# Kernel tuning notes

Measured on AMD Instinct MI355X. Metric: run time of the kernel, lower is better.

## Reference

```python
import jax, jax.numpy as jnp
import numpy as np

EMB = 1024
HEADS = 16
HEAD_SIZE = EMB // HEADS
B, T = 2, 2048


def setup_inputs() -> dict:
    key = jax.random.key(0)
    k1, k2, k3 = jax.random.split(key, 3)
    scale = 0.02
    x = jax.random.normal(k1, (B, T, EMB), dtype=jnp.float32)
    w_qkv = jax.random.normal(k2, (3 * EMB, EMB), dtype=jnp.float32) * scale  # torch Linear weight [out,in]
    w_out = jax.random.normal(k3, (EMB, EMB), dtype=jnp.float32) * scale
    return {"x": x, "w_qkv": w_qkv, "w_out": w_out}


def reference(x, w_qkv, w_out):
    Bx, Tx, C = x.shape
    att_scale = 1.0 / np.sqrt(HEAD_SIZE).astype(np.float32)
    qkv = x @ w_qkv.T  # [B,T,3C]
    q, k, v = jnp.split(qkv, 3, axis=-1)
    # [B,T,H,Dh] -> [B,H,T,Dh]
    q = q.reshape(Bx, Tx, HEADS, HEAD_SIZE).transpose(0, 2, 1, 3)
    k = k.reshape(Bx, Tx, HEADS, HEAD_SIZE).transpose(0, 2, 1, 3)
    v = v.reshape(Bx, Tx, HEADS, HEAD_SIZE).transpose(0, 2, 1, 3)
    att = jnp.einsum('bhqd,bhkd->bhqk', q, k) * att_scale
    causal = jnp.tril(jnp.ones((Tx, Tx), dtype=bool))  # True = keep
    att = jnp.where(causal[None, None], att, jnp.finfo(att.dtype).min)
    att = jax.nn.softmax(att, axis=-1)
    y = jnp.einsum('bhqk,bhkd->bhqd', att, v)
    y = y.transpose(0, 2, 1, 3).reshape(Bx, Tx, C)
    return y @ w_out.T
```

## Files before the change

### kernel.cpp

```cpp
#include <hip/hip_runtime.h>
#include <hip/hip_bf16.h>
#include <cstdint>


typedef __bf16 bf16x8 __attribute__((ext_vector_type(8)));
typedef float  f32x4  __attribute__((ext_vector_type(4)));
typedef unsigned short u16x4 __attribute__((ext_vector_type(4)));

#define EMB   1024
#define HEADS 16
#define HD    64
#define TT    2048
#define NROWS 4096
#define QKVN  3072
#define SCL   0.18033688f
#define THR   11.0f

__global__ void cvt_all(const float* __restrict__ x, const float* __restrict__ wq,
                        const float* __restrict__ wo, __bf16* __restrict__ xb,
                        __bf16* __restrict__ wqb, __bf16* __restrict__ wob) {
  const int bid = blockIdx.x;
  const float* in; __bf16* out; int i;
  if (bid < 2048)      { in = x;  out = xb;  i = bid * 256 + threadIdx.x; }
  else if (bid < 3584) { in = wq; out = wqb; i = (bid - 2048) * 256 + threadIdx.x; }
  else                 { in = wo; out = wob; i = (bid - 3584) * 256 + threadIdx.x; }
  const float4* p = (const float4*)in + (size_t)i * 2;
  float4 a = p[0], b = p[1];
  bf16x8 o;
  o[0] = (__bf16)a.x; o[1] = (__bf16)a.y; o[2] = (__bf16)a.z; o[3] = (__bf16)a.w;
  o[4] = (__bf16)b.x; o[5] = (__bf16)b.y; o[6] = (__bf16)b.z; o[7] = (__bf16)b.w;
  *((bf16x8*)out + i) = o;
}

__device__ __forceinline__ void gload_lds16(const void* g, void* l) {
  __builtin_amdgcn_global_load_lds(
      (const __attribute__((address_space(1))) void*)(uintptr_t)g,
      (__attribute__((address_space(3))) void*)(uint32_t)(uintptr_t)l,
      16, 0, 0);
}

template <int MODE>
__global__ __launch_bounds__(256, 2)
void gemm_bt(const __bf16* __restrict__ A, const __bf16* __restrict__ Bm,
             void* __restrict__ Cout, __bf16* __restrict__ vt,
             int M, int N, int K) {
  __shared__ __align__(16) char As[128 * 128];
  __shared__ __align__(16) char Bs[128 * 128];
  const int tid  = threadIdx.x;
  const int lane = tid & 63;
  const int wid  = tid >> 6;
  const int wr = wid >> 1, wc = wid & 1;
  const int nwg = gridDim.x * gridDim.y;
  int flat = blockIdx.y * gridDim.x + blockIdx.x;
  flat = (flat & 7) * (nwg >> 3) + (flat >> 3);
  const int brow = (flat / gridDim.x) * 128;
  const int bcol = (flat % gridDim.x) * 128;
  const int fr = lane & 15, g = lane >> 4;

  f32x4 acc[4][4];
#pragma unroll
  for (int m = 0; m < 4; m++)
#pragma unroll
    for (int n = 0; n < 4; n++)
#pragma unroll
      for (int r = 0; r < 4; r++) acc[m][n][r] = 0.0f;

  for (int k0 = 0; k0 < K; k0 += 64) {
    __syncthreads();
#pragma unroll
    for (int i = 0; i < 4; i++) {
      const int c = tid + i * 256;
      const int row = c >> 3, pos = c & 7;
      const int sc = pos ^ (row & 7);
      gload_lds16(A  + (size_t)(brow + row) * K + k0 + sc * 8, As + c * 16);
      gload_lds16(Bm + (size_t)(bcol + row) * K + k0 + sc * 8, Bs + c * 16);
    }
    __syncthreads();

    bf16x8 af[4][2], bfr[4][2];
#pragma unroll
    for (int m = 0; m < 4; m++)
#pragma unroll
      for (int kc = 0; kc < 2; kc++) {
        const int row = wr * 64 + m * 16 + fr;
        af[m][kc] = *(const bf16x8*)(As + row * 128 + (((kc << 2) | g) ^ (fr & 7)) * 16);
      }
#pragma unroll
    for (int n = 0; n < 4; n++)
#pragma unroll
      for (int kc = 0; kc < 2; kc++) {
        const int row = wc * 64 + n * 16 + fr;
        bfr[n][kc] = *(const bf16x8*)(Bs + row * 128 + (((kc << 2) | g) ^ (fr & 7)) * 16);
      }
#pragma unroll
    for (int kc = 0; kc < 2; kc++)
#pragma unroll
      for (int m = 0; m < 4; m++)
#pragma unroll
        for (int n = 0; n < 4; n++)
          acc[m][n] = __builtin_amdgcn_mfma_f32_16x16x32_bf16(af[m][kc], bfr[n][kc], acc[m][n], 0, 0, 0);
  }

  const int rbase = brow + wr * 64 + g * 4;
  const int cbase = bcol + wc * 64 + fr;
  if (MODE == 0) {
#pragma unroll
    for (int m = 0; m < 4; m++)
#pragma unroll
      for (int n = 0; n < 4; n++) {
        const int col = cbase + n * 16;
#pragma unroll
        for (int r = 0; r < 4; r++)
          ((float*)Cout)[(size_t)(rbase + m * 16 + r) * N + col] = acc[m][n][r];
      }
  } else if (bcol < 2 * EMB) {
    const float qscale = (bcol < EMB) ? SCL : 1.0f;
#pragma unroll
    for (int m = 0; m < 4; m++)
#pragma unroll
      for (int n = 0; n < 4; n++) {
        const int col = cbase + n * 16;
#pragma unroll
        for (int r = 0; r < 4; r++)
          ((__bf16*)Cout)[(size_t)(rbase + m * 16 + r) * N + col] = (__bf16)(acc[m][n][r] * qscale);
      }
  } else {
#pragma unroll
    for (int m = 0; m < 4; m++) {
      const int row0 = rbase + m * 16;
      const int b = row0 >> 11, t0 = row0 & 2047;
#pragma unroll
      for (int n = 0; n < 4; n++) {
        const int vcol = cbase + n * 16 - 2 * EMB;
        const int bh = b * HEADS + (vcol >> 6);
        const int d  = vcol & 63;
        u16x4 pk;
#pragma unroll
        for (int r = 0; r < 4; r++) {
          const __bf16 h = (__bf16)acc[m][n][r];
          pk[r] = *(const unsigned short*)&h;
        }
        *(u16x4*)(vt + ((size_t)bh * HD + d) * TT + t0) = pk;
      }
    }
  }
}

__device__ __forceinline__ int psw(int row) {
  return (((row & 7) ^ ((row >> 3) & 7))) << 4;
}

__global__ __launch_bounds__(256, 2)
void attn_causal9(const __bf16* __restrict__ qkv, const __bf16* __restrict__ vt,
                  __bf16* __restrict__ yb) {
  __shared__ __align__(16) char Kbuf[4][8192];
  __shared__ __align__(16) char Vbuf[4][8192];
  __shared__ __align__(16) char Pbuf[4][2048];

  const int tid = threadIdx.x;
  const int lane = tid & 63, w = tid >> 6;
  const int L = blockIdx.x;
  const int bh = L & 31;
  const int chunk = 31 - (L >> 5);
  const int b = bh >> 4, h = bh & 15;
  const size_t rowbase = (size_t)b * TT;
  const int q0 = chunk * 64 + w * 16;
  const int fr = lane & 15, g = lane >> 4;
  const int ntiles = chunk + 1;

  bf16x8 qf[2];
#pragma unroll
  for (int kc = 0; kc < 2; kc++)
    qf[kc] = *(const bf16x8*)(qkv + (rowbase + q0 + fr) * QKVN + h * HD + kc * 32 + g * 8);

  bf16x8 ones;
#pragma unroll
  for (int j = 0; j < 8; j++) ones[j] = (__bf16)1.0f;

  f32x4 o[4];
  f32x4 lacc;
  float m[4];
#pragma unroll
  for (int n = 0; n < 4; n++)
#pragma unroll
    for (int r = 0; r < 4; r++) o[n][r] = 0.0f;
#pragma unroll
  for (int r = 0; r < 4; r++) { lacc[r] = 0.0f; m[r] = -1e30f; }

  auto stageKV = [&](int kt, int buf) {
#pragma unroll
    for (int i = 0; i < 2; i++) {
      const int c = tid + i * 256;
      const int row = c >> 3;
      const int c16 = (c & 7) ^ (row & 7);
      gload_lds16(qkv + (rowbase + kt * 64 + row) * QKVN + EMB + h * HD + c16 * 8,
                  Kbuf[buf] + c * 16);
    }
#pragma unroll
    for (int i = 0; i < 2; i++) {
      const int c = tid + i * 256;
      const int row = c >> 3;
      const int c16 = (c & 7) ^ (row & 7);
      gload_lds16(vt + ((size_t)bh * HD + row) * TT + kt * 64 + c16 * 8,
                  Vbuf[buf] + c * 16);
    }
  };

  auto doQK = [&](int kt, f32x4 (&s)[4]) {
    const char* Kc = Kbuf[kt & 3];
    bf16x8 kf[4][2];
#pragma unroll
    for (int n = 0; n < 4; n++)
#pragma unroll
      for (int kc = 0; kc < 2; kc++) {
        const int row = n * 16 + fr;
        kf[n][kc] = *(const bf16x8*)(Kc + row * 128 + (((kc << 2) | g) ^ (row & 7)) * 16);
      }
#pragma unroll
    for (int n = 0; n < 4; n++) {
#pragma unroll
      for (int r = 0; r < 4; r++) s[n][r] = 0.0f;
#pragma unroll
      for (int kc = 0; kc < 2; kc++)
        s[n] = __builtin_amdgcn_mfma_f32_16x16x32_bf16(qf[kc], kf[n][kc], s[n], 0, 0, 0);
    }
  };

  auto doSoftmax = [&](int kt, f32x4 (&s)[4]) {
    const int kv0 = kt * 64;
    if (kt == chunk) {
#pragma unroll
      for (int n = 0; n < 4; n++)
#pragma unroll
        for (int r = 0; r < 4; r++) {
          const int qg = q0 + g * 4 + r;
          const int kg = kv0 + n * 16 + fr;
          if (kg > qg) s[n][r] = -1e30f;
        }
    }
    float pm[4];
#pragma unroll
    for (int r = 0; r < 4; r++)
      pm[r] = fmaxf(fmaxf(s[0][r], s[1][r]), fmaxf(s[2][r], s[3][r]));
    const bool ok = (pm[0] <= m[0] + THR) && (pm[1] <= m[1] + THR) &&
                    (pm[2] <= m[2] + THR) && (pm[3] <= m[3] + THR);
    if (!__all(ok)) {
#pragma unroll
      for (int r = 0; r < 4; r++) {
        float rm = pm[r];
#pragma unroll
        for (int d = 1; d < 16; d <<= 1) rm = fmaxf(rm, __shfl_xor(rm, d, 16));
        const float nm = fmaxf(m[r], rm);
        const float f = __builtin_amdgcn_exp2f(m[r] - nm);
        m[r] = nm;
        lacc[r] *= f;
#pragma unroll
        for (int n = 0; n < 4; n++) o[n][r] *= f;
      }
    }
#pragma unroll
    for (int n = 0; n < 4; n++)
#pragma unroll
      for (int r = 0; r < 4; r++) {
        const float e = __builtin_amdgcn_exp2f(s[n][r] - m[r]);
        const int row = g * 4 + r;
        *(__bf16*)(Pbuf[w] + row * 128 + (((n * 16 + fr) * 2) ^ psw(row))) = (__bf16)e;
      }
  };

  auto doPV = [&](int kt) {
    const char* Vc = Vbuf[kt & 3];
    bf16x8 pa[2];
#pragma unroll
    for (int kc = 0; kc < 2; kc++)
      pa[kc] = *(const bf16x8*)(Pbuf[w] + fr * 128 + ((kc * 64 + g * 16) ^ psw(fr)));
    bf16x8 vb[4][2];
#pragma unroll
    for (int n = 0; n < 4; n++)
#pragma unroll
      for (int kc = 0; kc < 2; kc++) {
        const int row = n * 16 + fr;
        vb[n][kc] = *(const bf16x8*)(Vc + row * 128 + (((kc << 2) | g) ^ (row & 7)) * 16);
      }
#pragma unroll
    for (int kc = 0; kc < 2; kc++) {
      lacc = __builtin_amdgcn_mfma_f32_16x16x32_bf16(pa[kc], ones, lacc, 0, 0, 0);
#pragma unroll
      for (int n = 0; n < 4; n++)
        o[n] = __builtin_amdgcn_mfma_f32_16x16x32_bf16(pa[kc], vb[n][kc], o[n], 0, 0, 0);
    }
  };

  stageKV(0, 0);
  if (ntiles > 1) stageKV(1, 1);
  if (ntiles > 2) stageKV(2, 2);
  if (ntiles > 2) asm volatile("s_waitcnt vmcnt(4)" ::: "memory");
  else            asm volatile("s_waitcnt vmcnt(0)" ::: "memory");
  __builtin_amdgcn_s_barrier();

  {
    f32x4 s0[4];
    doQK(0, s0);
    doSoftmax(0, s0);
  }

  for (int t = 0; t < ntiles; t++) {
    if (t + 3 < ntiles) stageKV(t + 3, (t + 3) & 3);

    const bool nxt = (t + 1 < ntiles);
    f32x4 s[4];
    if (nxt) doQK(t + 1, s);
    doPV(t);
    if (nxt) doSoftmax(t + 1, s);

    if (t + 3 < ntiles) asm volatile("s_waitcnt vmcnt(4)" ::: "memory");
    else                asm volatile("s_waitcnt vmcnt(0)" ::: "memory");
    __builtin_amdgcn_s_barrier();
  }

#pragma unroll
  for (int r = 0; r < 4; r++) {
    const float inv = __builtin_amdgcn_rcpf(lacc[r]);
#pragma unroll
    for (int n = 0; n < 4; n++) {
      const int q = q0 + g * 4 + r;
      const int d = n * 16 + fr;
      yb[(rowbase + q) * EMB + h * HD + d] = (__bf16)(o[n][r] * inv);
    }
  }
}

extern "C" void kernel_launch(void* const* d_in, const int* in_sizes, int n_in,
                              void* d_out, int out_size, void* d_ws, size_t ws_size,
                              hipStream_t stream) {
  const float* x     = (const float*)d_in[0];
  const float* w_qkv = (const float*)d_in[1];
  const float* w_out = (const float*)d_in[2];
  float* out = (float*)d_out;

  char* ws = (char*)d_ws;
  __bf16* xb    = (__bf16*)(ws);
  __bf16* wqkvb = (__bf16*)(ws + (8ull  << 20));
  __bf16* wob   = (__bf16*)(ws + (14ull << 20));
  __bf16* qkvb  = (__bf16*)(ws + (16ull << 20));
  __bf16* vtb   = (__bf16*)(ws + (40ull << 20));
  __bf16* yb    = xb;

  cvt_all<<<4096, 256, 0, stream>>>(x, w_qkv, w_out, xb, wqkvb, wob);
  gemm_bt<1><<<dim3(QKVN / 128, NROWS / 128), 256, 0, stream>>>(xb, wqkvb, qkvb, vtb, NROWS, QKVN, EMB);
  attn_causal9<<<1024, 256, 0, stream>>>(qkvb, vtb, yb);
  gemm_bt<0><<<dim3(EMB / 128, NROWS / 128), 256, 0, stream>>>(yb, wob, out, nullptr, NROWS, EMB, EMB);
}
```

Measured before the change: 102.4 us.

## Enlarge attention query tile to 128 rows with 32 rows per wave

Each attention block now handles 128 queries instead of 64, and each wave handles 32 query rows in two 16-row MFMA groups. Every K/V tile staged into LDS is therefore reused across twice as many queries, halving K/V traffic and the number of blocks. Waves whose rows end before the last tile skip the extra QK and PV work, and MFMA sections are wrapped in s_setprio. The cost is more registers per wave, a larger P buffer, fewer blocks (512) for the GPU, and more load imbalance across waves.

```diff
diff --git a/kernel.cpp b/kernel.cpp
--- a/kernel.cpp
+++ b/kernel.cpp
@@ -151,41 +151,47 @@
 }
 
 __global__ __launch_bounds__(256, 2)
-void attn_causal9(const __bf16* __restrict__ qkv, const __bf16* __restrict__ vt,
-                  __bf16* __restrict__ yb) {
+void attn_causal13(const __bf16* __restrict__ qkv, const __bf16* __restrict__ vt,
+                   __bf16* __restrict__ yb) {
   __shared__ __align__(16) char Kbuf[4][8192];
   __shared__ __align__(16) char Vbuf[4][8192];
-  __shared__ __align__(16) char Pbuf[4][2048];
+  __shared__ __align__(16) char Pbuf[4][4096];
 
   const int tid = threadIdx.x;
   const int lane = tid & 63, w = tid >> 6;
   const int L = blockIdx.x;
   const int bh = L & 31;
-  const int chunk = 31 - (L >> 5);
+  const int chunk = 15 - (L >> 5);
   const int b = bh >> 4, h = bh & 15;
   const size_t rowbase = (size_t)b * TT;
-  const int q0 = chunk * 64 + w * 16;
+  const int q0 = chunk * 128 + w * 32;
   const int fr = lane & 15, g = lane >> 4;
-  const int ntiles = chunk + 1;
-
-  bf16x8 qf[2];
-#pragma unroll
-  for (int kc = 0; kc < 2; kc++)
-    qf[kc] = *(const bf16x8*)(qkv + (rowbase + q0 + fr) * QKVN + h * HD + kc * 32 + g * 8);
+  const int ntiles = 2 * chunk + 2;
+  const int tmaxw = (q0 + 31) >> 6;
+
+  bf16x8 qf[2][2];
+#pragma unroll
+  for (int m2 = 0; m2 < 2; m2++)
+#pragma unroll
+    for (int kc = 0; kc < 2; kc++)
+      qf[m2][kc] = *(const bf16x8*)(qkv + (rowbase + q0 + m2 * 16 + fr) * QKVN + h * HD + kc * 32 + g * 8);
 
   bf16x8 ones;
 #pragma unroll
   for (int j = 0; j < 8; j++) ones[j] = (__bf16)1.0f;
 
-  f32x4 o[4];
-  f32x4 lacc;
-  float m[4];
-#pragma unroll
-  for (int n = 0; n < 4; n++)
-#pragma unroll
-    for (int r = 0; r < 4; r++) o[n][r] = 0.0f;
-#pragma unroll
-  for (int r = 0; r < 4; r++) { lacc[r] = 0.0f; m[r] = -1e30f; }
+  f32x4 o[2][4];
+  f32x4 lacc[2];
+  float m[2][4];
+#pragma unroll
+  for (int m2 = 0; m2 < 2; m2++) {
+#pragma unroll
+    for (int n = 0; n < 4; n++)
+#pragma unroll
+      for (int r = 0; r < 4; r++) o[m2][n][r] = 0.0f;
+#pragma unroll
+    for (int r = 0; r < 4; r++) { lacc[m2][r] = 0.0f; m[m2][r] = -1e30f; }
+  }
 
   auto stageKV = [&](int kt, int buf) {
 #pragma unroll
@@ -206,7 +212,7 @@
     }
   };
 
-  auto doQK = [&](int kt, f32x4 (&s)[4]) {
+  auto doQK = [&](int kt, f32x4 (&s)[2][4]) {
     const char* Kc = Kbuf[kt & 3];
     bf16x8 kf[4][2];
 #pragma unroll
@@ -216,64 +222,84 @@
         const int row = n * 16 + fr;
         kf[n][kc] = *(const bf16x8*)(Kc + row * 128 + (((kc << 2) | g) ^ (row & 7)) * 16);
       }
-#pragma unroll
-    for (int n = 0; n < 4; n++) {
-#pragma unroll
-      for (int r = 0; r < 4; r++) s[n][r] = 0.0f;
-#pragma unroll
-      for (int kc = 0; kc < 2; kc++)
-        s[n] = __builtin_amdgcn_mfma_f32_16x16x32_bf16(qf[kc], kf[n][kc], s[n], 0, 0, 0);
-    }
+    __builtin_amdgcn_s_setprio(1);
+#pragma unroll
+    for (int m2 = 0; m2 < 2; m2++)
+#pragma unroll
+      for (int n = 0; n < 4; n++) {
+#pragma unroll
+        for (int r = 0; r < 4; r++) s[m2][n][r] = 0.0f;
+#pragma unroll
+        for (int kc = 0; kc < 2; kc++)
+          s[m2][n] = __builtin_amdgcn_mfma_f32_16x16x32_bf16(qf[m2][kc], kf[n][kc], s[m2][n], 0, 0, 0);
+      }
+    __builtin_amdgcn_s_setprio(0);
   };
 
-  auto doSoftmax = [&](int kt, f32x4 (&s)[4]) {
+  auto doSoftmax = [&](int kt, f32x4 (&s)[2][4]) {
     const int kv0 = kt * 64;
-    if (kt == chunk) {
+    if (kt == tmaxw) {
+#pragma unroll
+      for (int m2 = 0; m2 < 2; m2++)
+#pragma unroll
+        for (int n = 0; n < 4; n++)
+#pragma unroll
+          for (int r = 0; r < 4; r++) {
+            const int qg = q0 + m2 * 16 + g * 4 + r;
+            const int kg = kv0 + n * 16 + fr;
+            if (kg > qg) s[m2][n][r] = -1e30f;
+          }
+    }
+    float pm[2][4];
+#pragma unroll
+    for (int m2 = 0; m2 < 2; m2++)
+#pragma unroll
+      for (int r = 0; r < 4; r++)
+        pm[m2][r] = fmaxf(fmaxf(s[m2][0][r], s[m2][1][r]), fmaxf(s[m2][2][r], s[m2][3][r]));
+    bool okl = true;
+#pragma unroll
+    for (int m2 = 0; m2 < 2; m2++)
+#pragma unroll
+      for (int r = 0; r < 4; r++)
+        okl = okl && (pm[m2][r] <= m[m2][r] + THR);
+    if (!__all(okl)) {
+#pragma unroll
+      for (int m2 = 0; m2 < 2; m2++)
+#pragma unroll
+        for (int r = 0; r < 4; r++) {
+          float rm = pm[m2][r];
+#pragma unroll
+          for (int d = 1; d < 16; d <<= 1) rm = fmaxf(rm, __shfl_xor(rm, d, 16));
+          const float nm = fmaxf(m[m2][r], rm);
+          const float f = __builtin_amdgcn_exp2f(m[m2][r] - nm);
+          m[m2][r] = nm;
+          lacc[m2][r] *= f;
+#pragma unroll
+          for (int n = 0; n < 4; n++) o[m2][n][r] *= f;
+        }
+    }
+#pragma unroll
+    for (int m2 = 0; m2 < 2; m2++)
 #pragma unroll
       for (int n = 0; n < 4; n++)
 #pragma unroll
         for (int r = 0; r < 4; r++) {
-          const int qg = q0 + g * 4 + r;
-          const int kg = kv0 + n * 16 + fr;
-          if (kg > qg) s[n][r] = -1e30f;
+          const float e = __builtin_amdgcn_exp2f(s[m2][n][r] - m[m2][r]);
+          const int row = m2 * 16 + g * 4 + r;
+          *(__bf16*)(Pbuf[w] + row * 128 + (((n * 16 + fr) * 2) ^ psw(row))) = (__bf16)e;
         }
-    }
-    float pm[4];
-#pragma unroll
-    for (int r = 0; r < 4; r++)
-      pm[r] = fmaxf(fmaxf(s[0][r], s[1][r]), fmaxf(s[2][r], s[3][r]));
-    const bool ok = (pm[0] <= m[0] + THR) && (pm[1] <= m[1] + THR) &&
-                    (pm[2] <= m[2] + THR) && (pm[3] <= m[3] + THR);
-    if (!__all(ok)) {
-#pragma unroll
-      for (int r = 0; r < 4; r++) {
-        float rm = pm[r];
-#pragma unroll
-        for (int d = 1; d < 16; d <<= 1) rm = fmaxf(rm, __shfl_xor(rm, d, 16));
-        const float nm = fmaxf(m[r], rm);
-        const float f = __builtin_amdgcn_exp2f(m[r] - nm);
-        m[r] = nm;
-        lacc[r] *= f;
-#pragma unroll
-        for (int n = 0; n < 4; n++) o[n][r] *= f;
-      }
-    }
-#pragma unroll
-    for (int n = 0; n < 4; n++)
-#pragma unroll
-      for (int r = 0; r < 4; r++) {
-        const float e = __builtin_amdgcn_exp2f(s[n][r] - m[r]);
-        const int row = g * 4 + r;
-        *(__bf16*)(Pbuf[w] + row * 128 + (((n * 16 + fr) * 2) ^ psw(row))) = (__bf16)e;
-      }
   };
 
   auto doPV = [&](int kt) {
     const char* Vc = Vbuf[kt & 3];
-    bf16x8 pa[2];
-#pragma unroll
-    for (int kc = 0; kc < 2; kc++)
-      pa[kc] = *(const bf16x8*)(Pbuf[w] + fr * 128 + ((kc * 64 + g * 16) ^ psw(fr)));
+    bf16x8 pa[2][2];
+#pragma unroll
+    for (int m2 = 0; m2 < 2; m2++)
+#pragma unroll
+      for (int kc = 0; kc < 2; kc++) {
+        const int row = m2 * 16 + fr;
+        pa[m2][kc] = *(const bf16x8*)(Pbuf[w] + row * 128 + ((kc * 64 + g * 16) ^ psw(row)));
+      }
     bf16x8 vb[4][2];
 #pragma unroll
     for (int n = 0; n < 4; n++)
@@ -282,13 +308,17 @@
         const int row = n * 16 + fr;
         vb[n][kc] = *(const bf16x8*)(Vc + row * 128 + (((kc << 2) | g) ^ (row & 7)) * 16);
       }
-#pragma unroll
-    for (int kc = 0; kc < 2; kc++) {
-      lacc = __builtin_amdgcn_mfma_f32_16x16x32_bf16(pa[kc], ones, lacc, 0, 0, 0);
-#pragma unroll
-      for (int n = 0; n < 4; n++)
-        o[n] = __builtin_amdgcn_mfma_f32_16x16x32_bf16(pa[kc], vb[n][kc], o[n], 0, 0, 0);
-    }
+    __builtin_amdgcn_s_setprio(1);
+#pragma unroll
+    for (int m2 = 0; m2 < 2; m2++)
+#pragma unroll
+      for (int kc = 0; kc < 2; kc++) {
+        lacc[m2] = __builtin_amdgcn_mfma_f32_16x16x32_bf16(pa[m2][kc], ones, lacc[m2], 0, 0, 0);
+#pragma unroll
+        for (int n = 0; n < 4; n++)
+          o[m2][n] = __builtin_amdgcn_mfma_f32_16x16x32_bf16(pa[m2][kc], vb[n][kc], o[m2][n], 0, 0, 0);
+      }
+    __builtin_amdgcn_s_setprio(0);
   };
 
   stageKV(0, 0);
@@ -299,7 +329,7 @@
   __builtin_amdgcn_s_barrier();
 
   {
-    f32x4 s0[4];
+    f32x4 s0[2][4];
     doQK(0, s0);
     doSoftmax(0, s0);
   }
@@ -307,10 +337,10 @@
   for (int t = 0; t < ntiles; t++) {
     if (t + 3 < ntiles) stageKV(t + 3, (t + 3) & 3);
 
-    const bool nxt = (t + 1 < ntiles);
-    f32x4 s[4];
+    const bool nxt = (t + 1 < ntiles) && (t + 1 <= tmaxw);
+    f32x4 s[2][4];
     if (nxt) doQK(t + 1, s);
-    doPV(t);
+    if (t <= tmaxw) doPV(t);
     if (nxt) doSoftmax(t + 1, s);
 
     if (t + 3 < ntiles) asm volatile("s_waitcnt vmcnt(4)" ::: "memory");
@@ -319,15 +349,17 @@
   }
 
 #pragma unroll
-  for (int r = 0; r < 4; r++) {
-    const float inv = __builtin_amdgcn_rcpf(lacc[r]);
-#pragma unroll
-    for (int n = 0; n < 4; n++) {
-      const int q = q0 + g * 4 + r;
-      const int d = n * 16 + fr;
-      yb[(rowbase + q) * EMB + h * HD + d] = (__bf16)(o[n][r] * inv);
-    }
-  }
+  for (int m2 = 0; m2 < 2; m2++)
+#pragma unroll
+    for (int r = 0; r < 4; r++) {
+      const float inv = __builtin_amdgcn_rcpf(lacc[m2][r]);
+      const int q = q0 + m2 * 16 + g * 4 + r;
+#pragma unroll
+      for (int n = 0; n < 4; n++) {
+        const int d = n * 16 + fr;
+        yb[(rowbase + q) * EMB + h * HD + d] = (__bf16)(o[m2][n][r] * inv);
+      }
+    }
 }
 
 extern "C" void kernel_launch(void* const* d_in, const int* in_sizes, int n_in,
@@ -348,6 +380,6 @@
 
   cvt_all<<<4096, 256, 0, stream>>>(x, w_qkv, w_out, xb, wqkvb, wob);
   gemm_bt<1><<<dim3(QKVN / 128, NROWS / 128), 256, 0, stream>>>(xb, wqkvb, qkvb, vtb, NROWS, QKVN, EMB);
-  attn_causal9<<<1024, 256, 0, stream>>>(qkvb, vtb, yb);
+  attn_causal13<<<512, 256, 0, stream>>>(qkvb, vtb, yb);
   gemm_bt<0><<<dim3(EMB / 128, NROWS / 128), 256, 0, stream>>>(yb, wob, out, nullptr, NROWS, EMB, EMB);
 }
```

Result: slower. 111.6 us (+9.0%).

## Transpose attention MFMAs to keep P in registers and drop LDS round-trip

Applied to the files above, without the earlier changes.

Swaps the MFMA operand order so the score tile is computed transposed (keys along rows, queries along lanes). This turns the row max and sum into per-lane reductions plus two cross-lane shuffles. P is packed to bf16 and redistributed with shuffles instead of being written to and read back from an LDS buffer. The ones-MFMA for the row sum and per-row state are replaced by scalar accumulators, s_setprio is added around MFMA blocks, and the output is staged through LDS for 16-byte coalesced stores. The trade-off is extra shuffle and pack work in exchange for removing LDS traffic and MFMA work.

```diff
diff --git a/kernel.cpp b/kernel.cpp
--- a/kernel.cpp
+++ b/kernel.cpp
@@ -6,6 +6,7 @@
 typedef __bf16 bf16x8 __attribute__((ext_vector_type(8)));
 typedef float  f32x4  __attribute__((ext_vector_type(4)));
 typedef unsigned short u16x4 __attribute__((ext_vector_type(4)));
+typedef unsigned int   u32x4 __attribute__((ext_vector_type(4)));
 
 #define EMB   1024
 #define HEADS 16
@@ -150,12 +151,18 @@
   return (((row & 7) ^ ((row >> 3) & 7))) << 4;
 }
 
+__device__ __forceinline__ unsigned int pack_bf16(float a, float b) {
+  const __bf16 ha = (__bf16)a, hb = (__bf16)b;
+  const unsigned short ua = *(const unsigned short*)&ha;
+  const unsigned short ub = *(const unsigned short*)&hb;
+  return (unsigned int)ua | ((unsigned int)ub << 16);
+}
+
 __global__ __launch_bounds__(256, 2)
-void attn_causal9(const __bf16* __restrict__ qkv, const __bf16* __restrict__ vt,
-                  __bf16* __restrict__ yb) {
+void attn_causal15(const __bf16* __restrict__ qkv, const __bf16* __restrict__ vt,
+                   __bf16* __restrict__ yb) {
   __shared__ __align__(16) char Kbuf[4][8192];
   __shared__ __align__(16) char Vbuf[4][8192];
-  __shared__ __align__(16) char Pbuf[4][2048];
 
   const int tid = threadIdx.x;
   const int lane = tid & 63, w = tid >> 6;
@@ -173,19 +180,13 @@
   for (int kc = 0; kc < 2; kc++)
     qf[kc] = *(const bf16x8*)(qkv + (rowbase + q0 + fr) * QKVN + h * HD + kc * 32 + g * 8);
 
-  bf16x8 ones;
-#pragma unroll
-  for (int j = 0; j < 8; j++) ones[j] = (__bf16)1.0f;
-
   f32x4 o[4];
-  f32x4 lacc;
-  float m[4];
+  float lacc = 0.0f;
+  float ml = -1e30f;
 #pragma unroll
   for (int n = 0; n < 4; n++)
 #pragma unroll
     for (int r = 0; r < 4; r++) o[n][r] = 0.0f;
-#pragma unroll
-  for (int r = 0; r < 4; r++) { lacc[r] = 0.0f; m[r] = -1e30f; }
 
   auto stageKV = [&](int kt, int buf) {
 #pragma unroll
@@ -216,64 +217,83 @@
         const int row = n * 16 + fr;
         kf[n][kc] = *(const bf16x8*)(Kc + row * 128 + (((kc << 2) | g) ^ (row & 7)) * 16);
       }
+    __builtin_amdgcn_s_setprio(1);
 #pragma unroll
     for (int n = 0; n < 4; n++) {
 #pragma unroll
       for (int r = 0; r < 4; r++) s[n][r] = 0.0f;
 #pragma unroll
       for (int kc = 0; kc < 2; kc++)
-        s[n] = __builtin_amdgcn_mfma_f32_16x16x32_bf16(qf[kc], kf[n][kc], s[n], 0, 0, 0);
-    }
+        s[n] = __builtin_amdgcn_mfma_f32_16x16x32_bf16(kf[n][kc], qf[kc], s[n], 0, 0, 0);
+    }
+    __builtin_amdgcn_s_setprio(0);
   };
 
-  auto doSoftmax = [&](int kt, f32x4 (&s)[4]) {
+  auto doSM = [&](int kt, f32x4 (&s)[4], bf16x8 (&pb)[2]) {
     const int kv0 = kt * 64;
     if (kt == chunk) {
+      const int qg = q0 + fr;
 #pragma unroll
       for (int n = 0; n < 4; n++)
 #pragma unroll
         for (int r = 0; r < 4; r++) {
-          const int qg = q0 + g * 4 + r;
-          const int kg = kv0 + n * 16 + fr;
+          const int kg = kv0 + n * 16 + g * 4 + r;
           if (kg > qg) s[n][r] = -1e30f;
         }
     }
-    float pm[4];
-#pragma unroll
-    for (int r = 0; r < 4; r++)
-      pm[r] = fmaxf(fmaxf(s[0][r], s[1][r]), fmaxf(s[2][r], s[3][r]));
-    const bool ok = (pm[0] <= m[0] + THR) && (pm[1] <= m[1] + THR) &&
-                    (pm[2] <= m[2] + THR) && (pm[3] <= m[3] + THR);
-    if (!__all(ok)) {
+    float pm = s[0][0];
+#pragma unroll
+    for (int n = 0; n < 4; n++)
+#pragma unroll
+      for (int r = 0; r < 4; r++) pm = fmaxf(pm, s[n][r]);
+    pm = fmaxf(pm, __shfl_xor(pm, 16, 64));
+    pm = fmaxf(pm, __shfl_xor(pm, 32, 64));
+    if (!__all(pm <= ml + THR)) {
+      const float nm = fmaxf(ml, pm);
+      const float f = __builtin_amdgcn_exp2f(ml - nm);
+      ml = nm;
+      lacc *= f;
+#pragma unroll
+      for (int n = 0; n < 4; n++)
+#pragma unroll
+        for (int r = 0; r < 4; r++) o[n][r] *= f;
+    }
+    float p[4][4];
+    float ts = 0.0f;
+#pragma unroll
+    for (int n = 0; n < 4; n++)
 #pragma unroll
       for (int r = 0; r < 4; r++) {
-        float rm = pm[r];
-#pragma unroll
-        for (int d = 1; d < 16; d <<= 1) rm = fmaxf(rm, __shfl_xor(rm, d, 16));
-        const float nm = fmaxf(m[r], rm);
-        const float f = __builtin_amdgcn_exp2f(m[r] - nm);
-        m[r] = nm;
-        lacc[r] *= f;
-#pragma unroll
-        for (int n = 0; n < 4; n++) o[n][r] *= f;
-      }
-    }
-#pragma unroll
-    for (int n = 0; n < 4; n++)
-#pragma unroll
-      for (int r = 0; r < 4; r++) {
-        const float e = __builtin_amdgcn_exp2f(s[n][r] - m[r]);
-        const int row = g * 4 + r;
-        *(__bf16*)(Pbuf[w] + row * 128 + (((n * 16 + fr) * 2) ^ psw(row))) = (__bf16)e;
-      }
+        p[n][r] = __builtin_amdgcn_exp2f(s[n][r] - ml);
+        ts += p[n][r];
+      }
+    ts += __shfl_xor(ts, 16, 64);
+    ts += __shfl_xor(ts, 32, 64);
+    lacc += ts;
+    unsigned int pk[4][2];
+#pragma unroll
+    for (int n = 0; n < 4; n++)
+#pragma unroll
+      for (int w2 = 0; w2 < 2; w2++)
+        pk[n][w2] = pack_bf16(p[n][2 * w2], p[n][2 * w2 + 1]);
+    const int sl0 = fr + 16 * ((g & 1) * 2);
+    const int sl1 = sl0 + 16;
+#pragma unroll
+    for (int kc = 0; kc < 2; kc++) {
+      u32x4 bw;
+#pragma unroll
+      for (int ww = 0; ww < 4; ww++) {
+        const int src = (ww < 2) ? sl0 : sl1;
+        const unsigned int lo = (unsigned int)__shfl((int)pk[kc * 2][ww & 1], src, 64);
+        const unsigned int hi = (unsigned int)__shfl((int)pk[kc * 2 + 1][ww & 1], src, 64);
+        bw[ww] = (g & 2) ? hi : lo;
+      }
+      pb[kc] = *(bf16x8*)&bw;
+    }
   };
 
-  auto doPV = [&](int kt) {
+  auto doPV = [&](int kt, bf16x8 (&pb)[2]) {
     const char* Vc = Vbuf[kt & 3];
-    bf16x8 pa[2];
-#pragma unroll
-    for (int kc = 0; kc < 2; kc++)
-      pa[kc] = *(const bf16x8*)(Pbuf[w] + fr * 128 + ((kc * 64 + g * 16) ^ psw(fr)));
     bf16x8 vb[4][2];
 #pragma unroll
     for (int n = 0; n < 4; n++)
@@ -282,13 +302,13 @@
         const int row = n * 16 + fr;
         vb[n][kc] = *(const bf16x8*)(Vc + row * 128 + (((kc << 2) | g) ^ (row & 7)) * 16);
       }
-#pragma unroll
-    for (int kc = 0; kc < 2; kc++) {
-      lacc = __builtin_amdgcn_mfma_f32_16x16x32_bf16(pa[kc], ones, lacc, 0, 0, 0);
+    __builtin_amdgcn_s_setprio(1);
+#pragma unroll
+    for (int kc = 0; kc < 2; kc++)
 #pragma unroll
       for (int n = 0; n < 4; n++)
-        o[n] = __builtin_amdgcn_mfma_f32_16x16x32_bf16(pa[kc], vb[n][kc], o[n], 0, 0, 0);
-    }
+        o[n] = __builtin_amdgcn_mfma_f32_16x16x32_bf16(vb[n][kc], pb[kc], o[n], 0, 0, 0);
+    __builtin_amdgcn_s_setprio(0);
   };
 
   stageKV(0, 0);
@@ -298,10 +318,11 @@
   else            asm volatile("s_waitcnt vmcnt(0)" ::: "memory");
   __builtin_amdgcn_s_barrier();
 
+  bf16x8 pb[2];
   {
     f32x4 s0[4];
     doQK(0, s0);
-    doSoftmax(0, s0);
+    doSM(0, s0, pb);
   }
 
   for (int t = 0; t < ntiles; t++) {
@@ -310,22 +331,30 @@
     const bool nxt = (t + 1 < ntiles);
     f32x4 s[4];
     if (nxt) doQK(t + 1, s);
-    doPV(t);
-    if (nxt) doSoftmax(t + 1, s);
+    doPV(t, pb);
+    if (nxt) doSM(t + 1, s, pb);
 
     if (t + 3 < ntiles) asm volatile("s_waitcnt vmcnt(4)" ::: "memory");
     else                asm volatile("s_waitcnt vmcnt(0)" ::: "memory");
     __builtin_amdgcn_s_barrier();
   }
 
-#pragma unroll
-  for (int r = 0; r < 4; r++) {
-    const float inv = __builtin_amdgcn_rcpf(lacc[r]);
-#pragma unroll
-    for (int n = 0; n < 4; n++) {
-      const int q = q0 + g * 4 + r;
-      const int d = n * 16 + fr;
-      yb[(rowbase + q) * EMB + h * HD + d] = (__bf16)(o[n][r] * inv);
+  {
+    char* Tw = (char*)Kbuf + w * 2048;
+    const float inv = __builtin_amdgcn_rcpf(lacc);
+#pragma unroll
+    for (int n = 0; n < 4; n++)
+#pragma unroll
+      for (int r = 0; r < 4; r++) {
+        const int d = n * 16 + g * 4 + r;
+        *(__bf16*)(Tw + fr * 128 + ((d * 2) ^ psw(fr))) = (__bf16)(o[n][r] * inv);
+      }
+#pragma unroll
+    for (int i = 0; i < 2; i++) {
+      const int c = lane + i * 64;
+      const int row = c >> 3, pos = c & 7;
+      const bf16x8 v = *(const bf16x8*)(Tw + row * 128 + ((pos * 16) ^ psw(row)));
+      *(bf16x8*)(yb + (rowbase + q0 + row) * EMB + h * HD + pos * 8) = v;
     }
   }
 }
@@ -348,6 +377,6 @@
 
   cvt_all<<<4096, 256, 0, stream>>>(x, w_qkv, w_out, xb, wqkvb, wob);
   gemm_bt<1><<<dim3(QKVN / 128, NROWS / 128), 256, 0, stream>>>(xb, wqkvb, qkvb, vtb, NROWS, QKVN, EMB);
-  attn_causal9<<<1024, 256, 0, stream>>>(qkvb, vtb, yb);
+  attn_causal15<<<1024, 256, 0, stream>>>(qkvb, vtb, yb);
   gemm_bt<0><<<dim3(EMB / 128, NROWS / 128), 256, 0, stream>>>(yb, wob, out, nullptr, NROWS, EMB, EMB);
 }
```

After: 111.3 us. 8.7% more time.
